# Optimization experiments

Hardware: AMD Instinct MI355X
Metric: run time of the kernel (lower is better)

The kernel has to match this reference:

```python
import jax, jax.numpy as jnp
import numpy as np

B, D, T = 16384, 1024, 128  # batch, embed_dim, num_degradation_types
V, L = 4, 3                 # variants per sample, degradations per variant


def setup_inputs() -> dict:
    key = jax.random.key(0)
    k1, k2, k3, k4 = jax.random.split(key, 4)
    clean_embeddings = jax.random.normal(k1, (B, D), dtype=jnp.float32)
    W = jax.random.normal(k2, (T, D), dtype=jnp.float32) * (1.0 / np.sqrt(D))
    b = jnp.zeros((T,), dtype=jnp.float32)
    deg_indices = jax.random.randint(k3, (B, V, L), 0, T, dtype=jnp.int32)
    deg_mask = jax.random.randint(k4, (B, V, L), 0, 2, dtype=jnp.int32)
    return {"clean_embeddings": clean_embeddings, "W": W, "b": b,
            "deg_indices": deg_indices, "deg_mask": deg_mask}


def reference(clean_embeddings, W, b, deg_indices, deg_mask):
    # Linear + softmax: [B, T]
    logits = jnp.einsum("bd,td->bt", clean_embeddings, W) + b
    probs = jax.nn.softmax(logits, axis=-1)
    # Gather probs at each (batch, label) pair: [B, V*L] -> [B, V, L]
    flat_idx = deg_indices.reshape(B, V * L)
    gathered = jnp.take_along_axis(probs, flat_idx, axis=1).reshape(B, V, L)
    # Masked sum over all labels of a sample, divided by max(num_variants, 1)=V
    per_sample = (gathered * deg_mask.astype(probs.dtype)).sum(axis=(1, 2)) / V
    return per_sample.sum() / B
```

## Files before the change

### kernel.cpp

```cpp
#include <hip/hip_runtime.h>

#define B_SIZE 16384
#define D_DIM  1024
#define T_DIM  128
#define VLn    12
#define BM     32
#define BK     64
#define NCHUNK (D_DIM / BK)
#define GRID   (B_SIZE / BM)
#define SL_STRIDE 132

typedef _Float16 half8  __attribute__((ext_vector_type(8)));
typedef __fp16   fp16x2 __attribute__((ext_vector_type(2)));
typedef float    f32x4  __attribute__((ext_vector_type(4)));

union Pack16 { fp16x2 h[4]; uint4 u; };
union BReg   { uint4 u; half8 h; };

__device__ __forceinline__ uint4 pack8(float4 v0, float4 v1) {
    Pack16 un;
    un.h[0] = __builtin_amdgcn_cvt_pkrtz(v0.x, v0.y);
    un.h[1] = __builtin_amdgcn_cvt_pkrtz(v0.z, v0.w);
    un.h[2] = __builtin_amdgcn_cvt_pkrtz(v1.x, v1.y);
    un.h[3] = __builtin_amdgcn_cvt_pkrtz(v1.z, v1.w);
    return un.u;
}

__global__ __launch_bounds__(256)
void conv_w(const float* __restrict__ W, uint4* __restrict__ Wf) {
    const int j    = blockIdx.x * 256 + threadIdx.x;
    const int kc   = j >> 10;
    const int r    = j & 1023;
    const int g    = r >> 6;
    const int lane = r & 63;
    const int ks = g >> 3, CT = g & 7;
    const int n = CT * 16 + (lane & 15);
    const int k = kc * 64 + ks * 32 + ((lane >> 4) << 3);
    const float* src = W + (size_t)n * D_DIM + k;
    const float4 v0 = *(const float4*)src;
    const float4 v1 = *(const float4*)(src + 4);
    Wf[j] = pack8(v0, v1);
}

__global__ __launch_bounds__(256, 4)
void qloss_kernel(const float* __restrict__ emb,
                  const uint4* __restrict__ Wf,
                  const float* __restrict__ bias,
                  const int*   __restrict__ didx,
                  const int*   __restrict__ dmsk,
                  float*       __restrict__ part)
{
    __shared__ __align__(16) unsigned char smem[16928];
    float* sL   = (float*)smem;
    float* sRed = (float*)(smem + 16896);

    const int t    = threadIdx.x;
    const int w    = t >> 6;
    const int lane = t & 63;
    const int m15  = lane & 15;
    const int quad = lane >> 4;
    const int r0   = blockIdx.x * BM;

    const int sg   = t >> 6, sl = t & 63;
    const int srow = (sg >> 1) * 16 + (sl & 15);
    const int skk  = (sg & 1) * 32 + ((sl >> 4) << 3);
    const float* aBase = emb + (size_t)(r0 + srow) * D_DIM + skk;

    const uint4* wBase = Wf + (size_t)(2 * w) * 64 + lane;

    f32x4 acc[2][2];
#pragma unroll
    for (int mt = 0; mt < 2; ++mt)
#pragma unroll
        for (int ct = 0; ct < 2; ++ct) acc[mt][ct] = (f32x4){0.f, 0.f, 0.f, 0.f};

    BReg bcur[4], bnx1[4], bnx2[4];
    {
        const float4 v0 = *(const float4*)(aBase);
        const float4 v1 = *(const float4*)(aBase + 4);
        *(uint4*)(smem + t * 16) = pack8(v0, v1);
#pragma unroll
        for (int ks = 0; ks < 2; ++ks)
#pragma unroll
            for (int j = 0; j < 2; ++j) {
                bcur[ks * 2 + j].u = wBase[(size_t)(ks * 8 + j) * 64];
                bnx1[ks * 2 + j].u = wBase[(size_t)1 * 1024 + (ks * 8 + j) * 64];
            }
    }
    __syncthreads();

#pragma unroll
    for (int kc = 0; kc < NCHUNK; ++kc) {
        unsigned char* sAc = smem + (kc & 1) * 4096;
        unsigned char* sAn = smem + ((kc & 1) ^ 1) * 4096;

        float4 va0, va1;
        if (kc + 1 < NCHUNK) {
            va0 = *(const float4*)(aBase + (kc + 1) * 64);
            va1 = *(const float4*)(aBase + (kc + 1) * 64 + 4);
        }
        if (kc + 2 < NCHUNK) {
#pragma unroll
            for (int ks = 0; ks < 2; ++ks)
#pragma unroll
                for (int j = 0; j < 2; ++j)
                    bnx2[ks * 2 + j].u =
                        wBase[(size_t)(kc + 2) * 1024 + (ks * 8 + j) * 64];
        }

#pragma unroll
        for (int ks = 0; ks < 2; ++ks) {
            const half8 a0 = *(const half8*)(sAc + ((0 * 2 + ks) * 64 + lane) * 16);
            const half8 a1 = *(const half8*)(sAc + ((1 * 2 + ks) * 64 + lane) * 16);
            acc[0][0] = __builtin_amdgcn_mfma_f32_16x16x32_f16(a0, bcur[ks * 2 + 0].h, acc[0][0], 0, 0, 0);
            acc[0][1] = __builtin_amdgcn_mfma_f32_16x16x32_f16(a0, bcur[ks * 2 + 1].h, acc[0][1], 0, 0, 0);
            acc[1][0] = __builtin_amdgcn_mfma_f32_16x16x32_f16(a1, bcur[ks * 2 + 0].h, acc[1][0], 0, 0, 0);
            acc[1][1] = __builtin_amdgcn_mfma_f32_16x16x32_f16(a1, bcur[ks * 2 + 1].h, acc[1][1], 0, 0, 0);
        }

        if (kc + 1 < NCHUNK)
            *(uint4*)(sAn + t * 16) = pack8(va0, va1);
#pragma unroll
        for (int q = 0; q < 4; ++q) { bcur[q] = bnx1[q]; bnx1[q] = bnx2[q]; }
        __syncthreads();
    }

    const int CT0 = w * 2;
    const float b0v = bias[CT0 * 16 + m15];
    const float b1v = bias[(CT0 + 1) * 16 + m15];
#pragma unroll
    for (int mt = 0; mt < 2; ++mt)
#pragma unroll
        for (int i = 0; i < 4; ++i) {
            const int row = mt * 16 + quad * 4 + i;
            sL[row * SL_STRIDE + CT0 * 16 + m15]       = acc[mt][0][i] + b0v;
            sL[row * SL_STRIDE + (CT0 + 1) * 16 + m15] = acc[mt][1][i] + b1v;
        }
    __syncthreads();

    {
        const int row = t >> 3, s = t & 7;
        float* base = &sL[row * SL_STRIDE + s * 16];
        float v[16];
#pragma unroll
        for (int j = 0; j < 4; ++j) *(float4*)&v[j * 4] = *(const float4*)(base + j * 4);
        float m = -1e30f;
#pragma unroll
        for (int j = 0; j < 16; ++j) m = fmaxf(m, v[j]);
#pragma unroll
        for (int off = 1; off < 8; off <<= 1) m = fmaxf(m, __shfl_xor(m, off));
        float ssum = 0.f;
#pragma unroll
        for (int j = 0; j < 16; ++j) { v[j] = __expf(v[j] - m); ssum += v[j]; }
#pragma unroll
        for (int off = 1; off < 8; off <<= 1) ssum += __shfl_xor(ssum, off);
        const float inv = 1.0f / ssum;
#pragma unroll
        for (int j = 0; j < 16; ++j) v[j] *= inv;
#pragma unroll
        for (int j = 0; j < 4; ++j) *(float4*)(base + j * 4) = *(const float4*)&v[j * 4];
    }
    __syncthreads();

    float p = 0.f;
#pragma unroll
    for (int i = t; i < BM * VLn; i += 256) {
        const int gi  = r0 * VLn + i;
        const int row = i / VLn;
        const int idx = didx[gi];
        const int mk  = dmsk[gi];
        p += mk ? sL[row * SL_STRIDE + idx] : 0.f;
    }
#pragma unroll
    for (int off = 1; off < 64; off <<= 1) p += __shfl_xor(p, off);
    if (lane == 0) sRed[w] = p;
    __syncthreads();
    if (t == 0) part[blockIdx.x] = sRed[0] + sRed[1] + sRed[2] + sRed[3];
}

__global__ __launch_bounds__(256)
void reduce_k(const float* __restrict__ part, float* __restrict__ out) {
    __shared__ float s[4];
    const int t = threadIdx.x;
    float p = part[t] + part[t + 256];
#pragma unroll
    for (int off = 1; off < 64; off <<= 1) p += __shfl_xor(p, off);
    if ((t & 63) == 0) s[t >> 6] = p;
    __syncthreads();
    if (t == 0) out[0] = (s[0] + s[1] + s[2] + s[3]) * (1.0f / 65536.0f);
}

extern "C" void kernel_launch(void* const* d_in, const int* in_sizes, int n_in,
                              void* d_out, int out_size, void* d_ws, size_t ws_size,
                              hipStream_t stream) {
    const float* emb  = (const float*)d_in[0];
    const float* W    = (const float*)d_in[1];
    const float* bias = (const float*)d_in[2];
    const int*   didx = (const int*)d_in[3];
    const int*   dmsk = (const int*)d_in[4];
    float* out = (float*)d_out;

    uint4* Wf   = (uint4*)d_ws;
    float* part = (float*)((char*)d_ws + 262144);

    conv_w<<<64, 256, 0, stream>>>(W, Wf);
    qloss_kernel<<<GRID, 256, 0, stream>>>(emb, Wf, bias, didx, dmsk, part);
    reduce_k<<<1, 256, 0, stream>>>(part, out);
}
```

Baseline: 115.5 us.

## Deepen A-tile prefetch to two chunks and fold final reduction into atomics

The embedding loads are now issued two K-chunks ahead and held in registers, so global latency has more time to hide behind the MFMA work. The barrier is moved to just after the shared-memory store. The separate reduction kernel is replaced by a per-block atomicAdd into the output, with a memset beforehand, which removes one launch. Launch bounds are relaxed from 4 to 2 waves per SIMD to make room for the extra prefetch registers, at the cost of possibly lower occupancy and a nondeterministic float summation order.

After: 114.6 us. Within noise of the previous version (-0.8%).

```diff
diff --git a/kernel.cpp b/kernel.cpp
--- a/kernel.cpp
+++ b/kernel.cpp
@@ -42,13 +42,13 @@
     Wf[j] = pack8(v0, v1);
 }
 
-__global__ __launch_bounds__(256, 4)
+__global__ __launch_bounds__(256, 2)
 void qloss_kernel(const float* __restrict__ emb,
                   const uint4* __restrict__ Wf,
                   const float* __restrict__ bias,
                   const int*   __restrict__ didx,
                   const int*   __restrict__ dmsk,
-                  float*       __restrict__ part)
+                  float*       __restrict__ out)
 {
     __shared__ __align__(16) unsigned char smem[16928];
     float* sL   = (float*)smem;
@@ -75,10 +75,12 @@
         for (int ct = 0; ct < 2; ++ct) acc[mt][ct] = (f32x4){0.f, 0.f, 0.f, 0.f};
 
     BReg bcur[4], bnx1[4], bnx2[4];
+    float4 an0, an1, af0, af1;
     {
         const float4 v0 = *(const float4*)(aBase);
         const float4 v1 = *(const float4*)(aBase + 4);
-        *(uint4*)(smem + t * 16) = pack8(v0, v1);
+        an0 = *(const float4*)(aBase + 64);
+        an1 = *(const float4*)(aBase + 68);
 #pragma unroll
         for (int ks = 0; ks < 2; ++ks)
 #pragma unroll
@@ -86,6 +88,7 @@
                 bcur[ks * 2 + j].u = wBase[(size_t)(ks * 8 + j) * 64];
                 bnx1[ks * 2 + j].u = wBase[(size_t)1 * 1024 + (ks * 8 + j) * 64];
             }
+        *(uint4*)(smem + t * 16) = pack8(v0, v1);
     }
     __syncthreads();
 
@@ -94,12 +97,9 @@
         unsigned char* sAc = smem + (kc & 1) * 4096;
         unsigned char* sAn = smem + ((kc & 1) ^ 1) * 4096;
 
-        float4 va0, va1;
-        if (kc + 1 < NCHUNK) {
-            va0 = *(const float4*)(aBase + (kc + 1) * 64);
-            va1 = *(const float4*)(aBase + (kc + 1) * 64 + 4);
-        }
         if (kc + 2 < NCHUNK) {
+            af0 = *(const float4*)(aBase + (kc + 2) * 64);
+            af1 = *(const float4*)(aBase + (kc + 2) * 64 + 4);
 #pragma unroll
             for (int ks = 0; ks < 2; ++ks)
 #pragma unroll
@@ -119,10 +119,12 @@
         }
 
         if (kc + 1 < NCHUNK)
-            *(uint4*)(sAn + t * 16) = pack8(va0, va1);
+            *(uint4*)(sAn + t * 16) = pack8(an0, an1);
+        __syncthreads();
+
+        an0 = af0; an1 = af1;
 #pragma unroll
         for (int q = 0; q < 4; ++q) { bcur[q] = bnx1[q]; bnx1[q] = bnx2[q]; }
-        __syncthreads();
     }
 
     const int CT0 = w * 2;
@@ -175,19 +177,8 @@
     for (int off = 1; off < 64; off <<= 1) p += __shfl_xor(p, off);
     if (lane == 0) sRed[w] = p;
     __syncthreads();
-    if (t == 0) part[blockIdx.x] = sRed[0] + sRed[1] + sRed[2] + sRed[3];
-}
-
-__global__ __launch_bounds__(256)
-void reduce_k(const float* __restrict__ part, float* __restrict__ out) {
-    __shared__ float s[4];
-    const int t = threadIdx.x;
-    float p = part[t] + part[t + 256];
-#pragma unroll
-    for (int off = 1; off < 64; off <<= 1) p += __shfl_xor(p, off);
-    if ((t & 63) == 0) s[t >> 6] = p;
-    __syncthreads();
-    if (t == 0) out[0] = (s[0] + s[1] + s[2] + s[3]) * (1.0f / 65536.0f);
+    if (t == 0)
+        atomicAdd(out, (sRed[0] + sRed[1] + sRed[2] + sRed[3]) * (1.0f / 65536.0f));
 }
 
 extern "C" void kernel_launch(void* const* d_in, const int* in_sizes, int n_in,
@@ -200,10 +191,9 @@
     const int*   dmsk = (const int*)d_in[4];
     float* out = (float*)d_out;
 
-    uint4* Wf   = (uint4*)d_ws;
-    float* part = (float*)((char*)d_ws + 262144);
+    uint4* Wf = (uint4*)d_ws;
 
+    hipMemsetAsync(out, 0, sizeof(float), stream);
     conv_w<<<64, 256, 0, stream>>>(W, Wf);
-    qloss_kernel<<<GRID, 256, 0, stream>>>(emb, Wf, bias, didx, dmsk, part);
-    reduce_k<<<1, 256, 0, stream>>>(part, out);
+    qloss_kernel<<<GRID, 256, 0, stream>>>(emb, Wf, bias, didx, dmsk, out);
 }
```
